# Kernel optimization log

Hardware: AMD Instinct MI355X
Metric: run time of the kernel (lower is better)

The kernel has to match this reference:

```python
import jax, jax.numpy as jnp
import numpy as np

T, B, D_IN, D_H, D_OUT, N_LAYERS = 512, 64, 512, 1024, 512, 2
LN_EPS = 1e-5


def _gru_layer(x_seq, h0, w_ih, w_hh, b_ih, b_hh):
    # x_seq: [T,B,D_in], h0: [B,H]; w_ih: [3H,D_in], w_hh: [3H,H]
    # Precompute input-side gate projections for all timesteps at once.
    xg = jnp.einsum('tbd,gd->tbg', x_seq, w_ih) + b_ih  # [T,B,3H]

    def step(h, xg_t):
        hg = h @ w_hh.T + b_hh                         # [B,3H]
        xr, xz, xn = jnp.split(xg_t, 3, axis=-1)
        hr, hz, hn = jnp.split(hg, 3, axis=-1)
        r = jax.nn.sigmoid(xr + hr)
        z = jax.nn.sigmoid(xz + hz)
        n = jnp.tanh(xn + r * hn)
        h_new = (1.0 - z) * n + z * h
        return h_new, h_new

    _, ys = jax.lax.scan(step, h0, xg)                 # ys: [T,B,H]
    return ys


def setup_inputs() -> dict:
    key = jax.random.key(0)
    ks = jax.random.split(key, 16)
    s_in = 1.0 / np.sqrt(D_H)
    inp = {
        'x': jax.random.normal(ks[0], (T, B, D_IN), dtype=jnp.float32),
        'h': jax.random.normal(ks[1], (N_LAYERS, B, D_H), dtype=jnp.float32),
        # GRU layer 0 (input dim D_IN)
        'w_ih0': jax.random.uniform(ks[2], (3 * D_H, D_IN), minval=-s_in, maxval=s_in),
        'w_hh0': jax.random.uniform(ks[3], (3 * D_H, D_H), minval=-s_in, maxval=s_in),
        'b_ih0': jax.random.uniform(ks[4], (3 * D_H,), minval=-s_in, maxval=s_in),
        'b_hh0': jax.random.uniform(ks[5], (3 * D_H,), minval=-s_in, maxval=s_in),
        # GRU layer 1 (input dim D_H)
        'w_ih1': jax.random.uniform(ks[6], (3 * D_H, D_H), minval=-s_in, maxval=s_in),
        'w_hh1': jax.random.uniform(ks[7], (3 * D_H, D_H), minval=-s_in, maxval=s_in),
        'b_ih1': jax.random.uniform(ks[8], (3 * D_H,), minval=-s_in, maxval=s_in),
        'b_hh1': jax.random.uniform(ks[9], (3 * D_H,), minval=-s_in, maxval=s_in),
        # LayerNorm
        'ln_gamma': jnp.ones((D_H,), dtype=jnp.float32),
        'ln_beta': jnp.zeros((D_H,), dtype=jnp.float32),
        # Output linear
        'ff_w': jax.random.uniform(ks[10], (D_OUT, D_H), minval=-s_in, maxval=s_in),
        'ff_b': jax.random.uniform(ks[11], (D_OUT,), minval=-s_in, maxval=s_in),
    }
    return inp


def reference(x, h, w_ih0, w_hh0, b_ih0, b_hh0, w_ih1, w_hh1, b_ih1, b_hh1,
              ln_gamma, ln_beta, ff_w, ff_b):
    y0 = _gru_layer(x, h[0], w_ih0, w_hh0, b_ih0, b_hh0)   # [T,B,H]
    y1 = _gru_layer(y0, h[1], w_ih1, w_hh1, b_ih1, b_hh1)  # [T,B,H]
    # LayerNorm over last dim
    mu = jnp.mean(y1, axis=-1, keepdims=True)
    var = jnp.mean(jnp.square(y1 - mu), axis=-1, keepdims=True)
    yn = (y1 - mu) * jax.lax.rsqrt(var + LN_EPS) * ln_gamma + ln_beta
    # Output projection
    out = jnp.einsum('tbh,oh->tbo', yn, ff_w) + ff_b       # [T,B,D_OUT]
    return out
```

## Files before the change

kernel.cpp:

```cpp
#include <hip/hip_runtime.h>

#define T_SEQ 512
#define BATCH 64
#define DIN0  512
#define D_H   1024
#define D_OUT 512
#define NBLK  256

typedef __attribute__((ext_vector_type(8))) short short8;
typedef __attribute__((ext_vector_type(4))) float f32x4;

__device__ inline float bf2f(unsigned short u) {
    unsigned x = ((unsigned)u) << 16;
    return __builtin_bit_cast(float, x);
}
__device__ inline unsigned short f2bf(float f) {
    unsigned x = __builtin_bit_cast(unsigned, f);
    unsigned r = (x + 0x7fffu + ((x >> 16) & 1u)) >> 16;
    return (unsigned short)r;
}
__device__ inline float fast_sigmoid(float x) { return 1.f / (1.f + __expf(-x)); }
__device__ inline float fast_tanh(float x) {
    float ax = fabsf(x);
    float t = __expf(-2.f * ax);
    float r = (1.f - t) / (1.f + t);
    return copysignf(r, x);
}

__device__ inline void async_ld16_cohere(const void* g, void* l) {
    __builtin_amdgcn_global_load_lds((const __attribute__((address_space(1))) void*)g,
                                     (__attribute__((address_space(3))) void*)l,
                                     16, 0, 17);
}
__device__ inline void store_u16_sc01(void* p, unsigned v) {
    asm volatile("global_store_short %0, %1, off sc0 sc1" :: "v"(p), "v"(v) : "memory");
}
__device__ inline short8 load16_sc01(const void* p) {
    short8 r;
    asm volatile("global_load_dwordx4 %0, %1, off sc0 sc1"
                 : "=&v"(r) : "v"(p) : "memory");
    return r;
}
__device__ inline short8 load16_sc01_wait(const void* p) {
    short8 r;
    asm volatile("global_load_dwordx4 %0, %1, off sc0 sc1\n\ts_waitcnt vmcnt(0)"
                 : "=&v"(r) : "v"(p) : "memory");
    return r;
}

__global__ void cast_kernel(const float* __restrict__ in, unsigned short* __restrict__ out, int n4) {
    int i = blockIdx.x * blockDim.x + threadIdx.x;
    int stride = gridDim.x * blockDim.x;
    for (; i < n4; i += stride) {
        float4 v = ((const float4*)in)[i];
        ushort4 o;
        o.x = f2bf(v.x); o.y = f2bf(v.y); o.z = f2bf(v.z); o.w = f2bf(v.w);
        ((ushort4*)out)[i] = o;
    }
}

template <int DIN, bool FULLZH>
__global__ __launch_bounds__(128, 1) void gru_scan(
    const unsigned short* __restrict__ xseq,
    const unsigned short* __restrict__ wih,
    const unsigned short* __restrict__ whh,
    const float* __restrict__ bih, const float* __restrict__ bhh,
    const float* __restrict__ h0,
    unsigned short* __restrict__ hbuf,
    unsigned short* __restrict__ Y,
    unsigned short* __restrict__ flags)
{
    extern __shared__ unsigned short lds[];
    constexpr int WX_BASE = FULLZH ? 65536 : 49152;

    const int tid  = threadIdx.x;
    const int lane = tid & 63;
    const int wv   = tid >> 6;
    const int bid  = blockIdx.x;
    const int xcd  = bid & 7;
    const int rg   = xcd >> 1;
    const int cb   = ((bid >> 3) << 1) | (xcd & 1);
    const int c0   = cb * 16, r0 = rg * 16;

    unsigned short* const frg = flags + rg * 64;

    {
        const int NG = FULLZH ? 3 : 2;
        for (int g = 0; g < NG; ++g) {
            const int grow = (g == 0) ? 2 * D_H : (g == 1 ? 0 : D_H);
            unsigned short* W = lds + 16384 + g * 16384;
            for (int i = tid; i < 16 * 128; i += 128) {
                int c = i >> 7, kb = i & 127;
                int el = (c * 1024 + kb * 8) ^ ((c & 7) << 3);
                *(short8*)&W[el] = *(const short8*)&whh[(size_t)(grow + c0 + c) * D_H + kb * 8];
            }
        }
        for (int g = 0; g < 2; ++g) {
            const int grow = (g == 0) ? 2 * D_H : 0;
            unsigned short* W = lds + WX_BASE + g * 16 * DIN;
            for (int i = tid; i < 16 * (DIN / 8); i += 128) {
                int c = i / (DIN / 8), kb = i % (DIN / 8);
                int el = (c * DIN + kb * 8) ^ ((c & 7) << 3);
                *(short8*)&W[el] = *(const short8*)&wih[(size_t)(grow + c0 + c) * DIN + kb * 8];
            }
        }
    }
    __syncthreads();

    const int gc   = c0 + (lane & 15);
    const int crow = (lane >> 4) * 4;
    float hprev[4];
    float b_r, b_z, b_xn, b_hn;
    if (wv == 0) {
        #pragma unroll
        for (int i = 0; i < 4; ++i) {
            float v = h0[(size_t)(r0 + crow + i) * D_H + gc];
            hprev[i] = v;
            store_u16_sc01(&hbuf[(size_t)(r0 + crow + i) * D_H + gc], (unsigned)f2bf(v));
        }
        asm volatile("s_waitcnt vmcnt(0)" ::: "memory");
        if (lane == 0) store_u16_sc01(&frg[cb], 1u);
        b_r  = bih[gc] + bhh[gc];
        b_z  = bih[D_H + gc] + bhh[D_H + gc];
        b_xn = bih[2 * D_H + gc];
        b_hn = bhh[2 * D_H + gc];
    }

    const int arow = lane & 15;
    const int ako  = (lane >> 4) * 8;
    const int swz  = (arow & 7) << 3;

    f32x4 fr, fz, fnx, fnh;

    for (int t = 0; t < T_SEQ; ++t) {
        const unsigned short* hb  = hbuf + (t & 1) * (BATCH * D_H);
        unsigned short*       hbn = hbuf + ((t & 1) ^ 1) * (BATCH * D_H);
        const unsigned short* xt  = xseq + (size_t)t * BATCH * DIN;
        unsigned short*       Yt  = Y + (size_t)t * BATCH * D_H;

        if (wv == 1) {
            const int p = t + 1;
            const unsigned short* fp = frg + (lane & 7) * 8;
            while (true) {
                short8 f = load16_sc01_wait(fp);
                bool ok = true;
                #pragma unroll
                for (int j = 0; j < 8; ++j)
                    ok &= ((unsigned short)f[j] >= (unsigned)p);
                if (__all(ok)) break;
            }
            #pragma unroll
            for (int i = 0; i < 32; ++i) {
                int row = i >> 1, hf = i & 1;
                int sw8 = row & 7;
                const unsigned short* src =
                    hb + (size_t)(r0 + row) * D_H + (hf * 64 + (lane ^ sw8)) * 8;
                async_ld16_cohere(src, &lds[row * 1024 + hf * 512]);
            }
            asm volatile("s_waitcnt vmcnt(0)" ::: "memory");
        } else {
            fr = (f32x4){0.f, 0.f, 0.f, 0.f}; fz = fr; fnx = fr; fnh = fr;
            #pragma unroll 4
            for (int k = 0; k < DIN; k += 32) {
                short8 a  = *(const short8*)&xt[(size_t)(r0 + arow) * DIN + k + ako];
                int el    = (arow * DIN + k + ako) ^ swz;
                short8 bn = *(const short8*)&lds[WX_BASE + el];
                short8 br = *(const short8*)&lds[WX_BASE + 16 * DIN + el];
                short8 bz = *(const short8*)&wih[(size_t)(D_H + c0 + arow) * DIN + k + ako];
                fr  = __builtin_amdgcn_mfma_f32_16x16x32_bf16(a, br, fr, 0, 0, 0);
                fz  = __builtin_amdgcn_mfma_f32_16x16x32_bf16(a, bz, fz, 0, 0, 0);
                fnx = __builtin_amdgcn_mfma_f32_16x16x32_bf16(a, bn, fnx, 0, 0, 0);
            }
        }
        __syncthreads();

        if (wv == 0) {
            #pragma unroll 4
            for (int k = 0; k < D_H; k += 32) {
                int sel   = (arow * 1024 + k + ako) ^ swz;
                short8 a  = *(const short8*)&lds[sel];
                int el    = (arow * 1024 + k + ako) ^ swz;
                short8 bn = *(const short8*)&lds[16384 + el];
                short8 br = *(const short8*)&lds[32768 + el];
                short8 bz;
                if (FULLZH) bz = *(const short8*)&lds[49152 + el];
                else        bz = *(const short8*)&whh[(size_t)(D_H + c0 + arow) * D_H + k + ako];
                fr  = __builtin_amdgcn_mfma_f32_16x16x32_bf16(a, br, fr, 0, 0, 0);
                fz  = __builtin_amdgcn_mfma_f32_16x16x32_bf16(a, bz, fz, 0, 0, 0);
                fnh = __builtin_amdgcn_mfma_f32_16x16x32_bf16(a, bn, fnh, 0, 0, 0);
            }

            unsigned short h16[4];
            #pragma unroll
            for (int i = 0; i < 4; ++i) {
                int rr = r0 + crow + i;
                float r = fast_sigmoid(fr[i] + b_r);
                float z = fast_sigmoid(fz[i] + b_z);
                float n = fast_tanh(fnx[i] + b_xn + r * (fnh[i] + b_hn));
                float hn = (1.f - z) * n + z * hprev[i];
                hprev[i] = hn;
                h16[i] = f2bf(hn);
                store_u16_sc01(&hbn[(size_t)rr * D_H + gc], (unsigned)h16[i]);
            }
            asm volatile("s_waitcnt vmcnt(0)" ::: "memory");
            if (lane == 0) store_u16_sc01(&frg[cb], (unsigned)(t + 2));
            #pragma unroll
            for (int i = 0; i < 4; ++i)
                Yt[(size_t)(r0 + crow + i) * D_H + gc] = h16[i];
        }
        __syncthreads();
    }
}

__global__ __launch_bounds__(256) void ln_proj(
    const unsigned short* __restrict__ y1,
    const float* __restrict__ gamma, const float* __restrict__ beta,
    const unsigned short* __restrict__ ffw,
    const float* __restrict__ ffb,
    float* __restrict__ out)
{
    __shared__ unsigned short ylds[16 * 1024];
    const int row0 = blockIdx.x * 16;
    const int tid = threadIdx.x;

    {
        const int rr = tid >> 4, l16 = tid & 15;
        const unsigned short* yrow = y1 + (size_t)(row0 + rr) * D_H;
        float s = 0.f, sq = 0.f;
        #pragma unroll
        for (int j8 = 0; j8 < 8; ++j8) {
            int k = l16 * 64 + j8 * 8;
            short8 v = *(const short8*)&yrow[k];
            int idx = (rr * 1024 + k) ^ ((rr & 7) << 3);
            *(short8*)&ylds[idx] = v;
            #pragma unroll
            for (int j = 0; j < 8; ++j) {
                float f = bf2f((unsigned short)v[j]);
                s += f; sq += f * f;
            }
        }
        #pragma unroll
        for (int o = 1; o < 16; o <<= 1) {
            s  += __shfl_xor(s, o, 64);
            sq += __shfl_xor(sq, o, 64);
        }
        float mu = s * (1.f / 1024.f);
        float var = sq * (1.f / 1024.f) - mu * mu;
        float rstd = rsqrtf(var + 1e-5f);
        #pragma unroll
        for (int j8 = 0; j8 < 8; ++j8) {
            int k = l16 * 64 + j8 * 8;
            int idx = (rr * 1024 + k) ^ ((rr & 7) << 3);
            short8 v = *(short8*)&ylds[idx];
            short8 o8;
            #pragma unroll
            for (int j = 0; j < 8; ++j) {
                float f = bf2f((unsigned short)v[j]);
                f = (f - mu) * rstd * gamma[k + j] + beta[k + j];
                o8[j] = (short)f2bf(f);
            }
            *(short8*)&ylds[idx] = o8;
        }
    }
    __syncthreads();

    const int w = tid >> 6, lane = tid & 63;
    const int cbase = w * 128;
    const int arow = lane & 15, ako = (lane >> 4) * 8;
    f32x4 acc[8] = {};
    for (int k = 0; k < D_H; k += 32) {
        int aidx = (arow * 1024 + k + ako) ^ ((arow & 7) << 3);
        short8 a = *(const short8*)&ylds[aidx];
        #pragma unroll
        for (int n = 0; n < 8; ++n) {
            int col = cbase + n * 16 + (lane & 15);
            short8 b = *(const short8*)&ffw[col * 1024 + k + ako];
            acc[n] = __builtin_amdgcn_mfma_f32_16x16x32_bf16(a, b, acc[n], 0, 0, 0);
        }
    }
    #pragma unroll
    for (int n = 0; n < 8; ++n) {
        int col = cbase + n * 16 + (lane & 15);
        float bb = ffb[col];
        #pragma unroll
        for (int i = 0; i < 4; ++i) {
            int rr = row0 + (lane >> 4) * 4 + i;
            out[(size_t)rr * D_OUT + col] = acc[n][i] + bb;
        }
    }
}

extern "C" void kernel_launch(void* const* d_in, const int* in_sizes, int n_in,
                              void* d_out, int out_size, void* d_ws, size_t ws_size,
                              hipStream_t stream) {
    const float* x     = (const float*)d_in[0];
    const float* h     = (const float*)d_in[1];
    const float* w_ih0 = (const float*)d_in[2];
    const float* w_hh0 = (const float*)d_in[3];
    const float* b_ih0 = (const float*)d_in[4];
    const float* b_hh0 = (const float*)d_in[5];
    const float* w_ih1 = (const float*)d_in[6];
    const float* w_hh1 = (const float*)d_in[7];
    const float* b_ih1 = (const float*)d_in[8];
    const float* b_hh1 = (const float*)d_in[9];
    const float* ln_g  = (const float*)d_in[10];
    const float* ln_b  = (const float*)d_in[11];
    const float* ff_w  = (const float*)d_in[12];
    const float* ff_b  = (const float*)d_in[13];
    float* out = (float*)d_out;

    char* ws = (char*)d_ws;
    size_t off = 0;
    auto alloc = [&](size_t bytes) {
        void* p = ws + off;
        off = (off + bytes + 255) & ~(size_t)255;
        return p;
    };
    unsigned short* x_bf   = (unsigned short*)alloc((size_t)T_SEQ * BATCH * DIN0 * 2);
    unsigned short* y1_bf  = (unsigned short*)alloc((size_t)T_SEQ * BATCH * D_H * 2);
    unsigned short* wih0_b = (unsigned short*)alloc((size_t)3 * D_H * DIN0 * 2);
    unsigned short* whh0_b = (unsigned short*)alloc((size_t)3 * D_H * D_H * 2);
    unsigned short* wih1_b = (unsigned short*)alloc((size_t)3 * D_H * D_H * 2);
    unsigned short* whh1_b = (unsigned short*)alloc((size_t)3 * D_H * D_H * 2);
    unsigned short* ffw_b  = (unsigned short*)alloc((size_t)D_OUT * D_H * 2);
    unsigned short* hbuf   = (unsigned short*)alloc((size_t)2 * BATCH * D_H * 2);
    unsigned short* flags  = (unsigned short*)alloc(2 * 4 * 64 * 2);
    if (off > ws_size) return;

    unsigned short* y0_bf = (unsigned short*)d_out;

    hipMemsetAsync(flags, 0, 2 * 4 * 64 * 2, stream);

    auto castl = [&](const float* src, unsigned short* dst, int n) {
        int n4 = n / 4;
        int blocks = (n4 + 255) / 256;
        if (blocks > 2048) blocks = 2048;
        hipLaunchKernelGGL(cast_kernel, dim3(blocks), dim3(256), 0, stream, src, dst, n4);
    };
    castl(x,     x_bf,   T_SEQ * BATCH * DIN0);
    castl(w_ih0, wih0_b, 3 * D_H * DIN0);
    castl(w_hh0, whh0_b, 3 * D_H * D_H);
    castl(w_ih1, wih1_b, 3 * D_H * D_H);
    castl(w_hh1, whh1_b, 3 * D_H * D_H);
    castl(ff_w,  ffw_b,  D_OUT * D_H);

    const int ldsb = 163840;
    hipFuncSetAttribute((const void*)&gru_scan<DIN0, true>,
                        hipFuncAttributeMaxDynamicSharedMemorySize, ldsb);
    hipFuncSetAttribute((const void*)&gru_scan<D_H, false>,
                        hipFuncAttributeMaxDynamicSharedMemorySize, ldsb);

    hipLaunchKernelGGL((gru_scan<DIN0, true>), dim3(NBLK), dim3(128), ldsb, stream,
        x_bf, wih0_b, whh0_b, b_ih0, b_hh0, h, hbuf, y0_bf, flags);
    hipLaunchKernelGGL((gru_scan<D_H, false>), dim3(NBLK), dim3(128), ldsb, stream,
        y0_bf, wih1_b, whh1_b, b_ih1, b_hh1, h + BATCH * D_H, hbuf, y1_bf,
        flags + 256);
    hipLaunchKernelGGL(ln_proj, dim3(T_SEQ * BATCH / 16), dim3(256), 0, stream,
        y1_bf, ln_g, ln_b, ffw_b, ff_b, out);
}
```

Baseline: 8.205 ms.

## Store recurrent hidden state in 16x16 tile layout with vector stores

The shared hidden-state exchange buffer is re-laid out so each block's 16x16 output tile is contiguous. Each wave now stages its new h values in LDS and writes them with 16-byte coherent stores instead of many 2-byte scattered stores. The next step's reads become straight contiguous async copies into LDS, and the MFMA A-operand indexing changes to match. The flag spin loop is also bounded and given an s_sleep, which may add wake-up latency and drops the previous swizzle, so LDS bank conflicts are possible.

```diff
diff --git a/kernel.cpp b/kernel.cpp
--- a/kernel.cpp
+++ b/kernel.cpp
@@ -6,6 +6,7 @@
 #define D_H   1024
 #define D_OUT 512
 #define NBLK  256
+#define BH    (BATCH * D_H)
 
 typedef __attribute__((ext_vector_type(8))) short short8;
 typedef __attribute__((ext_vector_type(4))) float f32x4;
@@ -35,11 +36,8 @@
 __device__ inline void store_u16_sc01(void* p, unsigned v) {
     asm volatile("global_store_short %0, %1, off sc0 sc1" :: "v"(p), "v"(v) : "memory");
 }
-__device__ inline short8 load16_sc01(const void* p) {
-    short8 r;
-    asm volatile("global_load_dwordx4 %0, %1, off sc0 sc1"
-                 : "=&v"(r) : "v"(p) : "memory");
-    return r;
+__device__ inline void store16_sc01(void* p, short8 v) {
+    asm volatile("global_store_dwordx4 %0, %1, off sc0 sc1" :: "v"(p), "v"(v) : "memory");
 }
 __device__ inline short8 load16_sc01_wait(const void* p) {
     short8 r;
@@ -81,6 +79,7 @@
     const int rg   = xcd >> 1;
     const int cb   = ((bid >> 3) << 1) | (xcd & 1);
     const int c0   = cb * 16, r0 = rg * 16;
+    const int tile = rg * 64 + cb;
 
     unsigned short* const frg = flags + rg * 64;
 
@@ -109,6 +108,9 @@
 
     const int gc   = c0 + (lane & 15);
     const int crow = (lane >> 4) * 4;
+    const int arow = lane & 15;
+    const int ako  = (lane >> 4) * 8;
+    const int swz  = (arow & 7) << 3;
     float hprev[4];
     float b_r, b_z, b_xn, b_hn;
     if (wv == 0) {
@@ -116,7 +118,7 @@
         for (int i = 0; i < 4; ++i) {
             float v = h0[(size_t)(r0 + crow + i) * D_H + gc];
             hprev[i] = v;
-            store_u16_sc01(&hbuf[(size_t)(r0 + crow + i) * D_H + gc], (unsigned)f2bf(v));
+            store_u16_sc01(&hbuf[tile * 256 + (crow + i) * 16 + arow], (unsigned)f2bf(v));
         }
         asm volatile("s_waitcnt vmcnt(0)" ::: "memory");
         if (lane == 0) store_u16_sc01(&frg[cb], 1u);
@@ -126,37 +128,29 @@
         b_hn = bhh[2 * D_H + gc];
     }
 
-    const int arow = lane & 15;
-    const int ako  = (lane >> 4) * 8;
-    const int swz  = (arow & 7) << 3;
-
     f32x4 fr, fz, fnx, fnh;
 
     for (int t = 0; t < T_SEQ; ++t) {
-        const unsigned short* hb  = hbuf + (t & 1) * (BATCH * D_H);
-        unsigned short*       hbn = hbuf + ((t & 1) ^ 1) * (BATCH * D_H);
-        const unsigned short* xt  = xseq + (size_t)t * BATCH * DIN;
-        unsigned short*       Yt  = Y + (size_t)t * BATCH * D_H;
+        const unsigned short* hbt  = hbuf + (t & 1) * BH + rg * 64 * 256;
+        unsigned short*       hbnt = hbuf + ((t & 1) ^ 1) * BH + tile * 256;
+        const unsigned short* xt   = xseq + (size_t)t * BATCH * DIN;
+        unsigned short*       Yt   = Y + (size_t)t * BATCH * D_H;
 
         if (wv == 1) {
             const int p = t + 1;
             const unsigned short* fp = frg + (lane & 7) * 8;
-            while (true) {
+            for (int it = 0; it < 200000; ++it) {
                 short8 f = load16_sc01_wait(fp);
                 bool ok = true;
                 #pragma unroll
                 for (int j = 0; j < 8; ++j)
                     ok &= ((unsigned short)f[j] >= (unsigned)p);
                 if (__all(ok)) break;
-            }
-            #pragma unroll
-            for (int i = 0; i < 32; ++i) {
-                int row = i >> 1, hf = i & 1;
-                int sw8 = row & 7;
-                const unsigned short* src =
-                    hb + (size_t)(r0 + row) * D_H + (hf * 64 + (lane ^ sw8)) * 8;
-                async_ld16_cohere(src, &lds[row * 1024 + hf * 512]);
-            }
+                __builtin_amdgcn_s_sleep(1);
+            }
+            #pragma unroll
+            for (int i = 0; i < 32; ++i)
+                async_ld16_cohere(hbt + i * 512 + lane * 8, &lds[i * 512]);
             asm volatile("s_waitcnt vmcnt(0)" ::: "memory");
         } else {
             fr = (f32x4){0.f, 0.f, 0.f, 0.f}; fz = fr; fnx = fr; fnh = fr;
@@ -177,7 +171,7 @@
         if (wv == 0) {
             #pragma unroll 4
             for (int k = 0; k < D_H; k += 32) {
-                int sel   = (arow * 1024 + k + ako) ^ swz;
+                int sel   = ((k + ako) >> 4) * 256 + arow * 16 + ((k + ako) & 15);
                 short8 a  = *(const short8*)&lds[sel];
                 int el    = (arow * 1024 + k + ako) ^ swz;
                 short8 bn = *(const short8*)&lds[16384 + el];
@@ -193,14 +187,17 @@
             unsigned short h16[4];
             #pragma unroll
             for (int i = 0; i < 4; ++i) {
-                int rr = r0 + crow + i;
                 float r = fast_sigmoid(fr[i] + b_r);
                 float z = fast_sigmoid(fz[i] + b_z);
                 float n = fast_tanh(fnx[i] + b_xn + r * (fnh[i] + b_hn));
                 float hn = (1.f - z) * n + z * hprev[i];
                 hprev[i] = hn;
                 h16[i] = f2bf(hn);
-                store_u16_sc01(&hbn[(size_t)rr * D_H + gc], (unsigned)h16[i]);
+                lds[(crow + i) * 16 + arow] = h16[i];
+            }
+            if (lane < 32) {
+                short8 val = *(const short8*)&lds[lane * 8];
+                store16_sc01(&hbnt[lane * 8], val);
             }
             asm volatile("s_waitcnt vmcnt(0)" ::: "memory");
             if (lane == 0) store_u16_sc01(&frg[cb], (unsigned)(t + 2));
@@ -323,7 +320,7 @@
     unsigned short* wih1_b = (unsigned short*)alloc((size_t)3 * D_H * D_H * 2);
     unsigned short* whh1_b = (unsigned short*)alloc((size_t)3 * D_H * D_H * 2);
     unsigned short* ffw_b  = (unsigned short*)alloc((size_t)D_OUT * D_H * 2);
-    unsigned short* hbuf   = (unsigned short*)alloc((size_t)2 * BATCH * D_H * 2);
+    unsigned short* hbuf   = (unsigned short*)alloc((size_t)2 * BH * 2);
     unsigned short* flags  = (unsigned short*)alloc(2 * 4 * 64 * 2);
     if (off > ws_size) return;
 
```

Measured after the change: 8.073 ms (median of 3 runs). No clear change (-1.6%).
